# Performance work log

Measured on AMD Instinct MI355X. Metric: run time of the kernel, lower is better.

## Reference

```python
import jax, jax.numpy as jnp
import numpy as np

NB_TASKS = 20
CLASSES_PER_TASK = 100  # uniform cfg.increments -> cache_repeat
TOPK = 2
TEMPERATURE = 5.0  # cfg.task_temperature


def setup_inputs() -> dict:
    key = jax.random.key(0)
    k1, k2, k3 = jax.random.split(key, 3)
    B = 8192
    N = NB_TASKS * CLASSES_PER_TASK
    return {
        "gol": jax.random.normal(k1, (B, NB_TASKS), dtype=jnp.float32),
        "gocls": jax.random.normal(k2, (B, N), dtype=jnp.float32),
        "do_logit": jax.random.normal(k3, (B, N), dtype=jnp.float32),
        "alpha": jnp.array([0.5], dtype=jnp.float32),
    }


def _masked(gol_use, do_logit):
    # mask_ = softmax(gol_use / T, dim=1).repeat_interleave(cache_repeat, dim=1)
    soft = jax.nn.softmax(gol_use / TEMPERATURE, axis=1)  # [B, T]
    # topk hard mask, scattered then repeated; hard*soft repeated == repeat(hard*soft)
    k = min(gol_use.shape[1], TOPK)
    _, tk = jax.lax.top_k(gol_use, k)  # [B, k] int indices
    B = gol_use.shape[0]
    hard = jnp.zeros_like(gol_use).at[jnp.arange(B)[:, None], tk].set(1.0)
    mask = jnp.repeat(hard * soft, CLASSES_PER_TASK, axis=1)  # [B, N]
    return do_logit * mask


def reference(gol, gocls, do_logit, alpha):
    B = gol.shape[0]
    # gocl = opt_by_task(gate_cls_logit, increments, 'amax'): per-task max over class logits
    gocl = gocls.reshape(B, NB_TASKS, CLASSES_PER_TASK).max(axis=-1)  # [B, T]
    logit_mcm = _masked(gol, do_logit)
    logit_gcl = _masked(gocl, do_logit)
    lamb = alpha  # broadcasts over [B, N]
    logit_mix = lamb * logit_mcm + (1.0 - lamb) * logit_gcl
    return logit_mix
```

## Files before the change

kernel.cpp:

```cpp
#include <hip/hip_runtime.h>
#include <hip/hip_bf16.h>
#include <math.h>

#define NB_TASKS 20
#define CLASSES_PER_TASK 100
#define N_COLS (NB_TASKS * CLASSES_PER_TASK)
#define INV_TEMP (1.0f / 5.0f)
#define ROWS_PER_BLOCK 4

__device__ __forceinline__ float rfl_f(float x) {
    return __int_as_float(__builtin_amdgcn_readfirstlane(__float_as_int(x)));
}

struct Top2 { int j1, j2; float w1, w2; };

__device__ __forceinline__ Top2 softmax_top2(float v, float coef, int lane) {
    float v1 = v; int i1 = lane;
    #pragma unroll
    for (int off = 16; off; off >>= 1) {
        float ov = __shfl_xor(v1, off);
        int   oj = __shfl_xor(i1, off);
        if (ov > v1 || (ov == v1 && oj < i1)) { v1 = ov; i1 = oj; }
    }
    float v2 = (lane == i1) ? -INFINITY : v;
    int   i2 = lane;
    #pragma unroll
    for (int off = 16; off; off >>= 1) {
        float ov = __shfl_xor(v2, off);
        int   oj = __shfl_xor(i2, off);
        if (ov > v2 || (ov == v2 && oj < i2)) { v2 = ov; i2 = oj; }
    }
    float ex  = __expf((v - v1) * INV_TEMP);
    float sum = ex;
    #pragma unroll
    for (int off = 16; off; off >>= 1)
        sum += __shfl_xor(sum, off);

    Top2 r;
    r.j1 = __builtin_amdgcn_readfirstlane(i1);
    r.j2 = __builtin_amdgcn_readfirstlane(i2);
    float w1 = coef / sum;
    float w2 = __expf((v2 - v1) * INV_TEMP) * w1;
    r.w1 = rfl_f(w1);
    r.w2 = rfl_f(w2);
    return r;
}

__global__ __launch_bounds__(256) void mix_kernel(
    const float* __restrict__ gol,
    const float* __restrict__ gocls,
    const float* __restrict__ dol,
    const float* __restrict__ alpha_p,
    float* __restrict__ out,
    int B)
{
    const int tid  = threadIdx.x;
    const int lane = tid & 63;
    const int b    = blockIdx.x * ROWS_PER_BLOCK + (tid >> 6);
    if (b >= B) return;

    const int grp = lane >> 4;
    const int s   = lane & 15;

    const float* grow = gocls + (size_t)b * N_COLS;

    const float a  = alpha_p[0];
    const float gv = (lane < NB_TASKS) ? gol[(size_t)b * NB_TASKS + lane] : -INFINITY;

    float cv = -INFINITY;
    #pragma unroll
    for (int k = 0; k < 5; ++k) {
        const float4* p = (const float4*)(grow + (4 * k + grp) * CLASSES_PER_TASK);
        float4 v0 = p[s];
        float m = fmaxf(fmaxf(v0.x, v0.y), fmaxf(v0.z, v0.w));
        if (s < 25 - 16) {
            float4 v1 = p[16 + s];
            m = fmaxf(m, fmaxf(fmaxf(v1.x, v1.y), fmaxf(v1.z, v1.w)));
        }
        #pragma unroll
        for (int off = 8; off; off >>= 1)
            m = fmaxf(m, __shfl_xor(m, off));
        float g2 = __shfl(m, (lane & 3) << 4);
        if ((lane >> 2) == k) cv = g2;
    }

    const Top2 pa = softmax_top2(gv, a,        lane);
    const Top2 pb = softmax_top2(cv, 1.0f - a, lane);

    const float4* din  = (const float4*)(dol + (size_t)b * N_COLS);
    float4*       dout = (float4*)(out + (size_t)b * N_COLS);

    #pragma unroll
    for (int i = 0; i < (N_COLS / 4 + 63) / 64; ++i) {
        const int f = lane + 64 * i;
        if (f < N_COLS / 4) {
            const int task = f / (CLASSES_PER_TASK / 4);
            float wgt = 0.0f;
            wgt += (task == pa.j1) ? pa.w1 : 0.0f;
            wgt += (task == pa.j2) ? pa.w2 : 0.0f;
            wgt += (task == pb.j1) ? pb.w1 : 0.0f;
            wgt += (task == pb.j2) ? pb.w2 : 0.0f;
            float4 r;
            if (wgt != 0.0f) {
                float4 v = din[f];
                r.x = v.x * wgt; r.y = v.y * wgt; r.z = v.z * wgt; r.w = v.w * wgt;
            } else {
                r.x = r.y = r.z = r.w = 0.0f;
            }
            dout[f] = r;
        }
    }
}

extern "C" void kernel_launch(void* const* d_in, const int* in_sizes, int n_in,
                              void* d_out, int out_size, void* d_ws, size_t ws_size,
                              hipStream_t stream) {
    const float* gol   = (const float*)d_in[0];
    const float* gocls = (const float*)d_in[1];
    const float* dol   = (const float*)d_in[2];
    const float* alpha = (const float*)d_in[3];
    float* out = (float*)d_out;

    const int B = in_sizes[0] / NB_TASKS;

    const int grid = (B + ROWS_PER_BLOCK - 1) / ROWS_PER_BLOCK;
    hipLaunchKernelGGL(mix_kernel, dim3(grid), dim3(256), 0, stream,
                       gol, gocls, dol, alpha, out, B);
}
```

Measured before the change: 28.18 us.

## Split gating weight computation and masked apply into two kernels

Splits the fused kernel into a weights kernel, which computes per-task mask weights and writes them to workspace, and an apply kernel, which reads the weights, broadcasts them by shuffle and scales do_logit with nontemporal stores. The aim is to decouple the latency-bound reduction and top-2 phase from the bandwidth-bound streaming phase, so the streaming kernel has less register pressure and can sustain more loads in flight. The cost is an extra launch, a small workspace round trip, and losing any overlap of the two phases inside one block.

```diff
diff --git a/kernel.cpp b/kernel.cpp
--- a/kernel.cpp
+++ b/kernel.cpp
@@ -5,8 +5,12 @@
 #define NB_TASKS 20
 #define CLASSES_PER_TASK 100
 #define N_COLS (NB_TASKS * CLASSES_PER_TASK)
+#define N_F4   (N_COLS / 4)
+#define F4_PER_TASK (CLASSES_PER_TASK / 4)
 #define INV_TEMP (1.0f / 5.0f)
 #define ROWS_PER_BLOCK 4
+
+typedef float vf4 __attribute__((ext_vector_type(4)));
 
 __device__ __forceinline__ float rfl_f(float x) {
     return __int_as_float(__builtin_amdgcn_readfirstlane(__float_as_int(x)));
@@ -46,12 +50,11 @@
     return r;
 }
 
-__global__ __launch_bounds__(256) void mix_kernel(
+__global__ __launch_bounds__(256) void weights_kernel(
     const float* __restrict__ gol,
     const float* __restrict__ gocls,
-    const float* __restrict__ dol,
     const float* __restrict__ alpha_p,
-    float* __restrict__ out,
+    float* __restrict__ wout,
     int B)
 {
     const int tid  = threadIdx.x;
@@ -70,11 +73,11 @@
     float cv = -INFINITY;
     #pragma unroll
     for (int k = 0; k < 5; ++k) {
-        const float4* p = (const float4*)(grow + (4 * k + grp) * CLASSES_PER_TASK);
-        float4 v0 = p[s];
+        const vf4* p = (const vf4*)(grow + (4 * k + grp) * CLASSES_PER_TASK);
+        vf4 v0 = p[s];
         float m = fmaxf(fmaxf(v0.x, v0.y), fmaxf(v0.z, v0.w));
         if (s < 25 - 16) {
-            float4 v1 = p[16 + s];
+            vf4 v1 = p[16 + s];
             m = fmaxf(m, fmaxf(fmaxf(v1.x, v1.y), fmaxf(v1.z, v1.w)));
         }
         #pragma unroll
@@ -87,27 +90,39 @@
     const Top2 pa = softmax_top2(gv, a,        lane);
     const Top2 pb = softmax_top2(cv, 1.0f - a, lane);
 
-    const float4* din  = (const float4*)(dol + (size_t)b * N_COLS);
-    float4*       dout = (float4*)(out + (size_t)b * N_COLS);
+    float w = 0.0f;
+    w += (lane == pa.j1) ? pa.w1 : 0.0f;
+    w += (lane == pa.j2) ? pa.w2 : 0.0f;
+    w += (lane == pb.j1) ? pb.w1 : 0.0f;
+    w += (lane == pb.j2) ? pb.w2 : 0.0f;
+
+    if (lane < NB_TASKS) wout[(size_t)b * NB_TASKS + lane] = w;
+}
+
+__global__ __launch_bounds__(256) void apply_kernel(
+    const float* __restrict__ win,
+    const float* __restrict__ dol,
+    float* __restrict__ out,
+    int B)
+{
+    const int tid  = threadIdx.x;
+    const int lane = tid & 63;
+    const int b    = blockIdx.x * ROWS_PER_BLOCK + (tid >> 6);
+    if (b >= B) return;
+
+    const float wv = (lane < NB_TASKS) ? win[(size_t)b * NB_TASKS + lane] : 0.0f;
+
+    const vf4* din  = (const vf4*)(dol + (size_t)b * N_COLS);
+    vf4*       dout = (vf4*)(out + (size_t)b * N_COLS);
 
     #pragma unroll
-    for (int i = 0; i < (N_COLS / 4 + 63) / 64; ++i) {
+    for (int i = 0; i < (N_F4 + 63) / 64; ++i) {
         const int f = lane + 64 * i;
-        if (f < N_COLS / 4) {
-            const int task = f / (CLASSES_PER_TASK / 4);
-            float wgt = 0.0f;
-            wgt += (task == pa.j1) ? pa.w1 : 0.0f;
-            wgt += (task == pa.j2) ? pa.w2 : 0.0f;
-            wgt += (task == pb.j1) ? pb.w1 : 0.0f;
-            wgt += (task == pb.j2) ? pb.w2 : 0.0f;
-            float4 r;
-            if (wgt != 0.0f) {
-                float4 v = din[f];
-                r.x = v.x * wgt; r.y = v.y * wgt; r.z = v.z * wgt; r.w = v.w * wgt;
-            } else {
-                r.x = r.y = r.z = r.w = 0.0f;
-            }
-            dout[f] = r;
+        if (f < N_F4) {
+            const float w = __shfl(wv, f / F4_PER_TASK);
+            vf4 r = {0.0f, 0.0f, 0.0f, 0.0f};
+            if (w != 0.0f) r = din[f] * w;
+            __builtin_nontemporal_store(r, &dout[f]);
         }
     }
 }
@@ -120,10 +135,13 @@
     const float* dol   = (const float*)d_in[2];
     const float* alpha = (const float*)d_in[3];
     float* out = (float*)d_out;
+    float* wbuf = (float*)d_ws;
 
     const int B = in_sizes[0] / NB_TASKS;
 
     const int grid = (B + ROWS_PER_BLOCK - 1) / ROWS_PER_BLOCK;
-    hipLaunchKernelGGL(mix_kernel, dim3(grid), dim3(256), 0, stream,
-                       gol, gocls, dol, alpha, out, B);
+    hipLaunchKernelGGL(weights_kernel, dim3(grid), dim3(256), 0, stream,
+                       gol, gocls, alpha, wbuf, B);
+    hipLaunchKernelGGL(apply_kernel, dim3(grid), dim3(256), 0, stream,
+                       wbuf, dol, out, B);
 }
```

After: 34.95 us. 24.0% more time.
